# Optimization experiments

Measured on AMD Instinct MI355X. Metric: run time of the kernel, lower is better.

## Reference

```python
import jax, jax.numpy as jnp
import numpy as np

N = 20000      # nodes
E = 320000     # edges per metapath graph
M = 3          # metapaths
IN = 256       # input feat dim
HID = 64       # num_hidden per head
NH = 4         # nhead (layer 1)
OUT = 256      # out_dim
NHO = 1        # nhead_out (layer 2)
SA_H = 128     # semantic attention hidden
NEG_SLOPE = 0.2


def gat_conv(h, W, attn_l, attn_r, src, dst, apply_relu):
    # h: [N, F_in]; W: [F_in, H*D]; attn_l/attn_r: [H, D]
    H, D = attn_l.shape
    feat = (h @ W).reshape(N, H, D)                      # [N, H, D]
    el = jnp.sum(feat * attn_l, axis=-1)                 # [N, H]
    er = jnp.sum(feat * attn_r, axis=-1)                 # [N, H]
    e = jax.nn.leaky_relu(el[src] + er[dst], NEG_SLOPE)  # [E, H]
    # edge softmax grouped by destination node
    emax = jax.ops.segment_max(e, dst, num_segments=N)   # [N, H] (-inf for empty)
    emax = jnp.where(jnp.isfinite(emax), emax, 0.0)
    ee = jnp.exp(e - emax[dst])                          # [E, H]
    denom = jax.ops.segment_sum(ee, dst, num_segments=N) # [N, H]
    alpha = ee / (denom[dst] + 1e-9)                     # [E, H]
    msg = alpha[:, :, None] * feat[src]                  # [E, H, D]
    out = jax.ops.segment_sum(msg, dst, num_segments=N)  # [N, H, D]
    out = out.reshape(N, H * D)                          # concat heads
    return jax.nn.relu(out) if apply_relu else out


def semantic_attention(z, W1, b1, v):
    # z: [N, M, F]
    w = jnp.tanh(z @ W1 + b1) @ v          # [N, M, 1]
    w = w.mean(axis=0)                     # [M, 1]
    beta = jax.nn.softmax(w, axis=0)       # [M, 1]
    out = jnp.sum(beta[None, :, :] * z, axis=1)  # [N, F]
    att_mp = beta.squeeze()                # [M]
    return out, att_mp


def setup_inputs() -> dict:
    key = jax.random.key(0)
    ks = jax.random.split(key, 16)
    s = 0.05
    return {
        "x": jax.random.normal(ks[0], (N, IN), dtype=jnp.float32),
        "edges": jax.random.randint(ks[1], (M, 2, E), 0, N, dtype=jnp.int64)
                 if jax.config.jax_enable_x64 else
                 jax.random.randint(ks[1], (M, 2, E), 0, N, dtype=jnp.int32),
        "W1": jax.random.normal(ks[2], (IN, NH * HID), dtype=jnp.float32) * s,
        "al1": jax.random.normal(ks[3], (NH, HID), dtype=jnp.float32) * s,
        "ar1": jax.random.normal(ks[4], (NH, HID), dtype=jnp.float32) * s,
        "saW1": jax.random.normal(ks[5], (NH * HID, SA_H), dtype=jnp.float32) * s,
        "sab1": jnp.zeros((SA_H,), dtype=jnp.float32),
        "sav1": jax.random.normal(ks[6], (SA_H, 1), dtype=jnp.float32) * s,
        "W2": jax.random.normal(ks[7], (NH * HID, NHO * OUT), dtype=jnp.float32) * s,
        "al2": jax.random.normal(ks[8], (NHO, OUT), dtype=jnp.float32) * s,
        "ar2": jax.random.normal(ks[9], (NHO, OUT), dtype=jnp.float32) * s,
        "saW2": jax.random.normal(ks[10], (NHO * OUT, SA_H), dtype=jnp.float32) * s,
        "sab2": jnp.zeros((SA_H,), dtype=jnp.float32),
        "sav2": jax.random.normal(ks[11], (SA_H, 1), dtype=jnp.float32) * s,
    }


def reference(x, edges, W1, al1, ar1, saW1, sab1, sav1,
              W2, al2, ar2, saW2, sab2, sav2):
    h = x
    # HAN layer 1: shared GATConv over each metapath graph, relu activation
    z = jnp.stack([gat_conv(h, W1, al1, ar1, edges[i, 0], edges[i, 1], True)
                   for i in range(M)], axis=1)          # [N, M, NH*HID]
    h, att_mp = semantic_attention(z, saW1, sab1, sav1)
    # HAN layer 2: last layer, no activation (encoding=False)
    z = jnp.stack([gat_conv(h, W2, al2, ar2, edges[i, 0], edges[i, 1], False)
                   for i in range(M)], axis=1)          # [N, M, NHO*OUT]
    h, att_mp = semantic_attention(z, saW2, sab2, sav2)
    return h, att_mp
```

## Files before the change

### kernel.cpp

```cpp
#include <hip/hip_runtime.h>
#include <hip/hip_bf16.h>
#include <math.h>

#define NN 20000
#define EE 320000
#define MM 3
#define FW 256
#define SAH 128
#define NB 79

typedef __attribute__((ext_vector_type(8))) short bf16x8;
typedef __attribute__((ext_vector_type(4))) float f32x4;

static __device__ __forceinline__ float lrelu(float x){ return x > 0.f ? x : 0.2f*x; }

static __device__ __forceinline__ unsigned short f2bf(float f) {
    unsigned u = __float_as_uint(f);
    return (unsigned short)((u + 0x7FFFu + ((u >> 16) & 1u)) >> 16);
}
static __device__ __forceinline__ float bflo(unsigned u){ return __uint_as_float(u << 16); }
static __device__ __forceinline__ float bfhi(unsigned u){ return __uint_as_float(u & 0xffff0000u); }
static __device__ __forceinline__ unsigned pk2bf(float lo, float hi) {
    return ((unsigned)f2bf(lo)) | (((unsigned)f2bf(hi)) << 16);
}

#define XBLK 2500
__global__ __launch_bounds__(256) void prep_kernel(const float* __restrict__ x, unsigned short* __restrict__ xb,
                                                   const float* __restrict__ W1, unsigned short* __restrict__ W1t,
                                                   const float* __restrict__ saW1, unsigned short* __restrict__ saW1t,
                                                   const float* __restrict__ W2, unsigned short* __restrict__ W2t,
                                                   const float* __restrict__ saW2, unsigned short* __restrict__ saW2t) {
    int b = blockIdx.x, tid = threadIdx.x;
    if (b < XBLK) {
        int i = b*256 + tid;
        const float4* p = (const float4*)x + (size_t)i*2;
        float4 v0 = p[0], v1 = p[1];
        uint4 o;
        o.x = pk2bf(v0.x, v0.y); o.y = pk2bf(v0.z, v0.w);
        o.z = pk2bf(v1.x, v1.y); o.w = pk2bf(v1.z, v1.w);
        ((uint4*)xb)[i] = o;
        return;
    }
    int b2 = b - XBLK;
    if (b2 < 256)      { int n = b2;       W1t  [(size_t)n*256 + tid] = f2bf(W1  [(size_t)tid*256 + n]); }
    else if (b2 < 384) { int n = b2 - 256; saW1t[(size_t)n*256 + tid] = f2bf(saW1[(size_t)tid*SAH + n]); }
    else if (b2 < 640) { int n = b2 - 384; W2t  [(size_t)n*256 + tid] = f2bf(W2  [(size_t)tid*256 + n]); }
    else               { int n = b2 - 640; saW2t[(size_t)n*256 + tid] = f2bf(saW2[(size_t)tid*SAH + n]); }
}

__global__ __launch_bounds__(256) void hist_kernel(const int* __restrict__ edges, int* __restrict__ cnt) {
    int idx = blockIdx.x*256 + threadIdx.x;
    if (idx >= MM*EE/4) return;
    int m = idx / (EE/4), e4 = idx - m*(EE/4);
    int4 d = ((const int4*)(edges + (size_t)(m*2+1)*EE))[e4];
    atomicAdd(&cnt[m*NN + d.x], 1);
    atomicAdd(&cnt[m*NN + d.y], 1);
    atomicAdd(&cnt[m*NN + d.z], 1);
    atomicAdd(&cnt[m*NN + d.w], 1);
}

__global__ __launch_bounds__(256) void scanA_kernel(const int* __restrict__ cnt, int* __restrict__ rowptr, int* __restrict__ bsum) {
    int m = blockIdx.y;
    int i = blockIdx.x*256 + threadIdx.x;
    int v = (i < NN) ? cnt[m*NN + i] : 0;
    int lane = threadIdx.x & 63;
    int val = v;
    #pragma unroll
    for (int o = 1; o < 64; o <<= 1) { int t = __shfl_up(val, o); if (lane >= o) val += t; }
    __shared__ int ws[4];
    int w = threadIdx.x >> 6;
    if (lane == 63) ws[w] = val;
    __syncthreads();
    #pragma unroll
    for (int j = 0; j < 3; ++j) if (j < w) val += ws[j];
    if (i < NN) rowptr[m*(NN+1) + 1 + i] = val;
    if (threadIdx.x == 255) bsum[m*NB + blockIdx.x] = val;
}

__global__ __launch_bounds__(128) void scanB_kernel(const int* __restrict__ bsum, int* __restrict__ boff) {
    __shared__ int s[128];
    int t = threadIdx.x;
    for (int m = 0; m < MM; ++m) {
        int v = (t < NB) ? bsum[m*NB + t] : 0;
        s[t] = v; __syncthreads();
        for (int o = 1; o < 128; o <<= 1) {
            int x = (t >= o) ? s[t - o] : 0;
            __syncthreads();
            s[t] += x;
            __syncthreads();
        }
        if (t < NB) boff[m*NB + t] = s[t] - v;
        __syncthreads();
    }
}

__global__ __launch_bounds__(256) void scanC_kernel(const int* __restrict__ cnt, int* __restrict__ rowptr,
                                                    const int* __restrict__ boff, int* __restrict__ cursor) {
    int m = blockIdx.y;
    int i = blockIdx.x*256 + threadIdx.x;
    if (i >= NN) return;
    int incl = rowptr[m*(NN+1) + 1 + i] + boff[m*NB + blockIdx.x];
    rowptr[m*(NN+1) + 1 + i] = incl;
    cursor[m*NN + i] = incl - cnt[m*NN + i];
    if (i == 0 && blockIdx.x == 0) rowptr[m*(NN+1)] = 0;
}

__global__ __launch_bounds__(256) void scatter_kernel(const int* __restrict__ edges, int* __restrict__ cursor,
                                                      uint2* __restrict__ csr) {
    int idx = blockIdx.x*256 + threadIdx.x;
    if (idx >= MM*EE/4) return;
    int m = idx / (EE/4), e4 = idx - m*(EE/4);
    int4 s = ((const int4*)(edges + (size_t)(m*2  )*EE))[e4];
    int4 d = ((const int4*)(edges + (size_t)(m*2+1)*EE))[e4];
    int p0 = atomicAdd(&cursor[m*NN + d.x], 1); csr[(size_t)m*EE + p0] = make_uint2((unsigned)s.x, (unsigned)d.x);
    int p1 = atomicAdd(&cursor[m*NN + d.y], 1); csr[(size_t)m*EE + p1] = make_uint2((unsigned)s.y, (unsigned)d.y);
    int p2 = atomicAdd(&cursor[m*NN + d.z], 1); csr[(size_t)m*EE + p2] = make_uint2((unsigned)s.z, (unsigned)d.z);
    int p3 = atomicAdd(&cursor[m*NN + d.w], 1); csr[(size_t)m*EE + p3] = make_uint2((unsigned)s.w, (unsigned)d.w);
}

template<int H>
__global__ __launch_bounds__(256) void gemm_mfma_kernel(const unsigned short* __restrict__ A,
                                                        const unsigned short* __restrict__ Bt,
                                                        const float* __restrict__ attl, const float* __restrict__ attr,
                                                        unsigned short* __restrict__ C,
                                                        float* __restrict__ el, float* __restrict__ er) {
    int tid = threadIdx.x;
    int w = tid >> 6, lane = tid & 63;
    int rowgrp = w & 1, half = w >> 1;
    int r0 = blockIdx.x*32 + rowgrp*16;
    int colbase = half * 128;
    int lrow = lane & 15, lk = lane >> 4;

    bf16x8 a[8];
    const unsigned short* ap = A + (size_t)(r0 + lrow)*256 + lk*8;
    #pragma unroll
    for (int k = 0; k < 8; ++k) a[k] = *(const bf16x8*)(ap + k*32);

    float pelv[2][4] = {{0.f,0.f,0.f,0.f},{0.f,0.f,0.f,0.f}};
    float perv[2][4] = {{0.f,0.f,0.f,0.f},{0.f,0.f,0.f,0.f}};

    #pragma unroll
    for (int n = 0; n < 8; ++n) {
        int col0 = colbase + n*16;
        const unsigned short* bp = Bt + (size_t)(col0 + lrow)*256 + lk*8;
        f32x4 acc = {0.f, 0.f, 0.f, 0.f};
        #pragma unroll
        for (int k = 0; k < 8; ++k) {
            bf16x8 bfr = *(const bf16x8*)(bp + k*32);
            acc = __builtin_amdgcn_mfma_f32_16x16x32_bf16(a[k], bfr, acc, 0, 0, 0);
        }
        int col = col0 + lrow;
        float al = attl[col], ar = attr[col];
        int hl = (H == 4) ? (n >> 2) : 0;
        #pragma unroll
        for (int r = 0; r < 4; ++r) {
            float cv = acc[r];
            pelv[hl][r] += cv * al;
            perv[hl][r] += cv * ar;
            C[(size_t)(r0 + lk*4 + r)*256 + col] = f2bf(cv);
        }
    }

    int nhl = (H == 4) ? 2 : 1;
    #pragma unroll
    for (int hl = 0; hl < 2; ++hl) {
        if (hl >= nhl) break;
        #pragma unroll
        for (int r = 0; r < 4; ++r) {
            float pe = pelv[hl][r], pr = perv[hl][r];
            #pragma unroll
            for (int o = 1; o < 16; o <<= 1) { pe += __shfl_xor(pe, o); pr += __shfl_xor(pr, o); }
            pelv[hl][r] = pe; perv[hl][r] = pr;
        }
    }

    if (H == 4) {
        if (lrow == 0) {
            int row = r0 + lk*4;
            #pragma unroll
            for (int hl = 0; hl < 2; ++hl) {
                int head = half*2 + hl;
                #pragma unroll
                for (int r = 0; r < 4; ++r) {
                    el[(size_t)(row + r)*4 + head] = pelv[hl][r];
                    er[(size_t)(row + r)*4 + head] = perv[hl][r];
                }
            }
        }
    } else {
        __shared__ float elds[2][32], erds[2][32];
        if (lrow == 0) {
            int rib = rowgrp*16 + lk*4;
            #pragma unroll
            for (int r = 0; r < 4; ++r) {
                elds[half][rib + r] = pelv[0][r];
                erds[half][rib + r] = perv[0][r];
            }
        }
        __syncthreads();
        if (tid < 32) {
            el[blockIdx.x*32 + tid] = elds[0][tid] + elds[1][tid];
            er[blockIdx.x*32 + tid] = erds[0][tid] + erds[1][tid];
        }
    }
}

template<int H>
__global__ __launch_bounds__(256) void edge_ee_kernel(const uint2* __restrict__ csr,
                                                      const float* __restrict__ el, const float* __restrict__ er,
                                                      float* __restrict__ ee) {
    int idx = blockIdx.x*256 + threadIdx.x;
    if (idx >= MM*EE) return;
    uint2 sd = csr[idx];
    int src = sd.x, dst = sd.y;
    if (H == 4) {
        float4 l = *(const float4*)&el[src*4];
        float4 r = *(const float4*)&er[dst*4];
        float4 s;
        s.x = expf(lrelu(l.x + r.x));
        s.y = expf(lrelu(l.y + r.y));
        s.z = expf(lrelu(l.z + r.z));
        s.w = expf(lrelu(l.w + r.w));
        *(float4*)&ee[(size_t)idx*4] = s;
    } else {
        ee[idx] = expf(lrelu(el[src] + er[dst]));
    }
}

template<int H, bool RELU>
__global__ __launch_bounds__(256) void agg_kernel(const unsigned short* __restrict__ feat,
                                                  const float* __restrict__ ee,
                                                  const int* __restrict__ rowptr,
                                                  const uint2* __restrict__ csr,
                                                  unsigned short* __restrict__ z) {
    int m = blockIdx.y;
    int tid = threadIdx.x;
    int lane = tid & 63, wv = tid >> 6;
    int n = blockIdx.x * 4 + wv;
    int eslot = lane >> 5, flane = lane & 31;
    int h = (H == 4) ? (flane >> 3) : 0;
    int beg = rowptr[m*(NN+1) + n], end = rowptr[m*(NN+1) + n + 1];
    const int eb = m*EE;

    float a[8] = {};
    float den = 0.f;
    int e0 = beg + eslot;

    int   sA = 0, sB = 0;
    float wA = 0.f, wB = 0.f;
    if (e0 < end)     { sA = csr[(size_t)eb+e0  ].x; wA = (H==4)? ee[(size_t)(eb+e0  )*4+h] : ee[eb+e0  ]; }
    if (e0 + 2 < end) { sB = csr[(size_t)eb+e0+2].x; wB = (H==4)? ee[(size_t)(eb+e0+2)*4+h] : ee[eb+e0+2]; }

    for (int e = e0; e < end; e += 2) {
        uint4 v = *(const uint4*)(feat + (size_t)sA*256 + flane*8);
        float w = wA;
        sA = sB; wA = wB;
        if (e + 4 < end) {
            sB = csr[(size_t)eb+e+4].x;
            wB = (H==4)? ee[(size_t)(eb+e+4)*4+h] : ee[eb+e+4];
        }
        den += w;
        a[0] += w * bflo(v.x); a[1] += w * bfhi(v.x);
        a[2] += w * bflo(v.y); a[3] += w * bfhi(v.y);
        a[4] += w * bflo(v.z); a[5] += w * bfhi(v.z);
        a[6] += w * bflo(v.w); a[7] += w * bfhi(v.w);
    }

    #pragma unroll
    for (int j = 0; j < 8; ++j) a[j] += __shfl_xor(a[j], 32);
    den += __shfl_xor(den, 32);

    if (eslot == 0) {
        float inv = 1.f / (den + 1e-9f);
        #pragma unroll
        for (int j = 0; j < 8; ++j) {
            a[j] *= inv;
            if (RELU) a[j] = fmaxf(a[j], 0.f);
        }
        uint4 pk;
        pk.x = pk2bf(a[0], a[1]);
        pk.y = pk2bf(a[2], a[3]);
        pk.z = pk2bf(a[4], a[5]);
        pk.w = pk2bf(a[6], a[7]);
        *(uint4*)&z[((size_t)n*MM + m)*256 + flane*8] = pk;
    }
}

__global__ __launch_bounds__(256) void semw_mfma_kernel(const unsigned short* __restrict__ Z,
                                                        const unsigned short* __restrict__ Wt,
                                                        const float* __restrict__ bias, const float* __restrict__ v,
                                                        float* __restrict__ wsum) {
    int tid = threadIdx.x;
    int w = tid >> 6, lane = tid & 63;
    int r0 = blockIdx.x*64 + w*16;
    int lrow = lane & 15, lk = lane >> 4;

    int arow = r0 + lrow;
    if (arow >= NN*MM) arow = NN*MM - 1;
    bf16x8 a[8];
    const unsigned short* ap = Z + (size_t)arow*256 + lk*8;
    #pragma unroll
    for (int k = 0; k < 8; ++k) a[k] = *(const bf16x8*)(ap + k*32);

    float p[4] = {0.f, 0.f, 0.f, 0.f};
    #pragma unroll
    for (int n = 0; n < 8; ++n) {
        int col = n*16 + lrow;
        const unsigned short* bp = Wt + (size_t)col*256 + lk*8;
        f32x4 acc = {0.f, 0.f, 0.f, 0.f};
        #pragma unroll
        for (int k = 0; k < 8; ++k) {
            bf16x8 bfr = *(const bf16x8*)(bp + k*32);
            acc = __builtin_amdgcn_mfma_f32_16x16x32_bf16(a[k], bfr, acc, 0, 0, 0);
        }
        float bb = bias[col], vv = v[col];
        #pragma unroll
        for (int r = 0; r < 4; ++r)
            p[r] += tanhf(acc[r] + bb) * vv;
    }

    #pragma unroll
    for (int r = 0; r < 4; ++r) {
        #pragma unroll
        for (int o = 1; o < 16; o <<= 1) p[r] += __shfl_xor(p[r], o);
    }

    __shared__ float loc[3];
    if (tid < 3) loc[tid] = 0.f;
    __syncthreads();
    if (lrow == 0) {
        #pragma unroll
        for (int r = 0; r < 4; ++r) {
            int row = r0 + lk*4 + r;
            if (row < NN*MM) atomicAdd(&loc[row % MM], p[r]);
        }
    }
    __syncthreads();
    if (tid < 3) atomicAdd(&wsum[tid], loc[tid]);
}

__global__ void beta_kernel(const float* __restrict__ wsum, float* __restrict__ beta, float* att_out) {
    if (threadIdx.x == 0 && blockIdx.x == 0) {
        float w0 = wsum[0] / (float)NN, w1 = wsum[1] / (float)NN, w2 = wsum[2] / (float)NN;
        float mx = fmaxf(w0, fmaxf(w1, w2));
        float e0 = expf(w0 - mx), e1 = expf(w1 - mx), e2 = expf(w2 - mx);
        float s = e0 + e1 + e2;
        beta[0] = e0 / s; beta[1] = e1 / s; beta[2] = e2 / s;
        if (att_out) { att_out[0] = e0/s; att_out[1] = e1/s; att_out[2] = e2/s; }
    }
}

__global__ __launch_bounds__(128) void combine_bf16_kernel(const unsigned short* __restrict__ z, const float* __restrict__ beta,
                                                           unsigned short* __restrict__ outb) {
    int n = blockIdx.x, t = threadIdx.x;
    float b0 = beta[0], b1 = beta[1], b2 = beta[2];
    size_t base = (size_t)n*MM*256 + t*2;
    unsigned z0 = *(const unsigned*)&z[base];
    unsigned z1 = *(const unsigned*)&z[base + 256];
    unsigned z2 = *(const unsigned*)&z[base + 512];
    float ox = b0*bflo(z0) + b1*bflo(z1) + b2*bflo(z2);
    float oy = b0*bfhi(z0) + b1*bfhi(z1) + b2*bfhi(z2);
    *(unsigned*)&outb[(size_t)n*256 + t*2] = pk2bf(ox, oy);
}

__global__ __launch_bounds__(128) void combine_kernel(const unsigned short* __restrict__ z, const float* __restrict__ beta,
                                                      float* __restrict__ out) {
    int n = blockIdx.x, t = threadIdx.x;
    float b0 = beta[0], b1 = beta[1], b2 = beta[2];
    size_t base = (size_t)n*MM*256 + t*2;
    unsigned z0 = *(const unsigned*)&z[base];
    unsigned z1 = *(const unsigned*)&z[base + 256];
    unsigned z2 = *(const unsigned*)&z[base + 512];
    float2 o;
    o.x = b0*bflo(z0) + b1*bflo(z1) + b2*bflo(z2);
    o.y = b0*bfhi(z0) + b1*bfhi(z1) + b2*bfhi(z2);
    *(float2*)&out[(size_t)n*256 + t*2] = o;
}

extern "C" void kernel_launch(void* const* d_in, const int* in_sizes, int n_in,
                              void* d_out, int out_size, void* d_ws, size_t ws_size,
                              hipStream_t stream) {
    const float* x    = (const float*)d_in[0];
    const int*   edges= (const int*)  d_in[1];
    const float* W1   = (const float*)d_in[2];
    const float* al1  = (const float*)d_in[3];
    const float* ar1  = (const float*)d_in[4];
    const float* saW1 = (const float*)d_in[5];
    const float* sab1 = (const float*)d_in[6];
    const float* sav1 = (const float*)d_in[7];
    const float* W2   = (const float*)d_in[8];
    const float* al2  = (const float*)d_in[9];
    const float* ar2  = (const float*)d_in[10];
    const float* saW2 = (const float*)d_in[11];
    const float* sab2 = (const float*)d_in[12];
    const float* sav2 = (const float*)d_in[13];
    float* out = (float*)d_out;

    char* ws = (char*)d_ws;
    size_t off = 0;
    auto alloc = [&](size_t bytes) { void* p = ws + off; off += (bytes + 255) & ~(size_t)255; return p; };
    unsigned short* feat  = (unsigned short*)alloc((size_t)NN*256*2);
    unsigned short* z     = (unsigned short*)alloc((size_t)NN*MM*256*2);
    unsigned short* xb    = (unsigned short*)alloc((size_t)NN*256*2);
    unsigned short* W1t   = (unsigned short*)alloc(256*256*2);
    unsigned short* saW1t = (unsigned short*)alloc(SAH*256*2);
    unsigned short* W2t   = (unsigned short*)alloc(256*256*2);
    unsigned short* saW2t = (unsigned short*)alloc(SAH*256*2);
    float* ee     = (float*)alloc((size_t)MM*EE*4*4);
    float* el     = (float*)alloc(NN*4*4);
    float* er     = (float*)alloc(NN*4*4);
    float* wsum   = (float*)alloc(256);
    float* beta   = (float*)alloc(256);
    int*   cnt    = (int*)alloc(MM*NN*4);
    int*   cursor = (int*)alloc(MM*NN*4);
    int*   rowptr = (int*)alloc(MM*(NN+1)*4);
    uint2* csr    = (uint2*)alloc((size_t)MM*EE*8);
    int*   bsum   = (int*)alloc(MM*NB*4);
    int*   boff   = (int*)alloc(MM*NB*4);
    unsigned short* hb = xb;

    int egrid = (MM*EE + 255)/256;
    int egrid4 = (MM*EE/4 + 255)/256;
    dim3 sg(NB, MM);

    prep_kernel<<<XBLK + 768, 256, 0, stream>>>(x, xb, W1, W1t, saW1, saW1t, W2, W2t, saW2, saW2t);

    hipMemsetAsync(cnt, 0, MM*NN*4, stream);
    hist_kernel<<<egrid4, 256, 0, stream>>>(edges, cnt);
    scanA_kernel<<<sg, 256, 0, stream>>>(cnt, rowptr, bsum);
    scanB_kernel<<<1, 128, 0, stream>>>(bsum, boff);
    scanC_kernel<<<sg, 256, 0, stream>>>(cnt, rowptr, boff, cursor);
    scatter_kernel<<<egrid4, 256, 0, stream>>>(edges, cursor, csr);

    gemm_mfma_kernel<4><<<NN/32, 256, 0, stream>>>(xb, W1t, al1, ar1, feat, el, er);
    edge_ee_kernel<4><<<egrid, 256, 0, stream>>>(csr, el, er, ee);
    agg_kernel<4, true><<<dim3(NN/4, MM), 256, 0, stream>>>(feat, ee, rowptr, csr, z);
    hipMemsetAsync(wsum, 0, 16, stream);
    semw_mfma_kernel<<<(NN*MM + 63)/64, 256, 0, stream>>>(z, saW1t, sab1, sav1, wsum);
    beta_kernel<<<1, 64, 0, stream>>>(wsum, beta, nullptr);
    combine_bf16_kernel<<<NN, 128, 0, stream>>>(z, beta, hb);

    gemm_mfma_kernel<1><<<NN/32, 256, 0, stream>>>(hb, W2t, al2, ar2, feat, el, er);
    edge_ee_kernel<1><<<egrid, 256, 0, stream>>>(csr, el, er, ee);
    agg_kernel<1, false><<<dim3(NN/4, MM), 256, 0, stream>>>(feat, ee, rowptr, csr, z);
    hipMemsetAsync(wsum, 0, 16, stream);
    semw_mfma_kernel<<<(NN*MM + 63)/64, 256, 0, stream>>>(z, saW2t, sab2, sav2, wsum);
    beta_kernel<<<1, 64, 0, stream>>>(wsum, beta, out + (size_t)NN*256);
    combine_kernel<<<NN, 128, 0, stream>>>(z, beta, out);
}
```

Before: 402.5 us.

## Store CSR as src-only, partition scatter by dst range, make edge_ee per-node

The CSR array now stores only source indices instead of (src,dst) pairs, which halves its memory traffic. The scatter kernel is split into 8 destination ranges so that each block's atomics and writes hit a narrower region and get better locality. This costs reading the edge list 8 times. The edge-weight kernel now walks each destination node's row, loading er once per node instead of once per edge. Warps can be underutilized because the average degree is only 16 while each wave has 64 lanes.

```diff
diff --git a/kernel.cpp b/kernel.cpp
--- a/kernel.cpp
+++ b/kernel.cpp
@@ -8,6 +8,7 @@
 #define FW 256
 #define SAH 128
 #define NB 79
+#define RNG 2500
 
 typedef __attribute__((ext_vector_type(8))) short bf16x8;
 typedef __attribute__((ext_vector_type(4))) float f32x4;
@@ -106,16 +107,19 @@
 }
 
 __global__ __launch_bounds__(256) void scatter_kernel(const int* __restrict__ edges, int* __restrict__ cursor,
-                                                      uint2* __restrict__ csr) {
-    int idx = blockIdx.x*256 + threadIdx.x;
-    if (idx >= MM*EE/4) return;
-    int m = idx / (EE/4), e4 = idx - m*(EE/4);
+                                                      int* __restrict__ csr_src) {
+    int m = blockIdx.y;
+    int r = blockIdx.x & 7;
+    int chunk = blockIdx.x >> 3;
+    int e4 = chunk*256 + threadIdx.x;
+    if (e4 >= EE/4) return;
+    int lo = r * RNG, hi = lo + RNG;
     int4 s = ((const int4*)(edges + (size_t)(m*2  )*EE))[e4];
     int4 d = ((const int4*)(edges + (size_t)(m*2+1)*EE))[e4];
-    int p0 = atomicAdd(&cursor[m*NN + d.x], 1); csr[(size_t)m*EE + p0] = make_uint2((unsigned)s.x, (unsigned)d.x);
-    int p1 = atomicAdd(&cursor[m*NN + d.y], 1); csr[(size_t)m*EE + p1] = make_uint2((unsigned)s.y, (unsigned)d.y);
-    int p2 = atomicAdd(&cursor[m*NN + d.z], 1); csr[(size_t)m*EE + p2] = make_uint2((unsigned)s.z, (unsigned)d.z);
-    int p3 = atomicAdd(&cursor[m*NN + d.w], 1); csr[(size_t)m*EE + p3] = make_uint2((unsigned)s.w, (unsigned)d.w);
+    if (d.x >= lo && d.x < hi) { int p = atomicAdd(&cursor[m*NN + d.x], 1); csr_src[(size_t)m*EE + p] = s.x; }
+    if (d.y >= lo && d.y < hi) { int p = atomicAdd(&cursor[m*NN + d.y], 1); csr_src[(size_t)m*EE + p] = s.y; }
+    if (d.z >= lo && d.z < hi) { int p = atomicAdd(&cursor[m*NN + d.z], 1); csr_src[(size_t)m*EE + p] = s.z; }
+    if (d.w >= lo && d.w < hi) { int p = atomicAdd(&cursor[m*NN + d.w], 1); csr_src[(size_t)m*EE + p] = s.w; }
 }
 
 template<int H>
@@ -206,24 +210,34 @@
 }
 
 template<int H>
-__global__ __launch_bounds__(256) void edge_ee_kernel(const uint2* __restrict__ csr,
+__global__ __launch_bounds__(256) void edge_ee_kernel(const int* __restrict__ csr_src,
+                                                      const int* __restrict__ rowptr,
                                                       const float* __restrict__ el, const float* __restrict__ er,
                                                       float* __restrict__ ee) {
-    int idx = blockIdx.x*256 + threadIdx.x;
-    if (idx >= MM*EE) return;
-    uint2 sd = csr[idx];
-    int src = sd.x, dst = sd.y;
+    int m = blockIdx.y;
+    int tid = threadIdx.x;
+    int lane = tid & 63, wv = tid >> 6;
+    int n = blockIdx.x*4 + wv;
+    int beg = rowptr[m*(NN+1) + n], end = rowptr[m*(NN+1) + n + 1];
+    const int eb = m*EE;
     if (H == 4) {
-        float4 l = *(const float4*)&el[src*4];
-        float4 r = *(const float4*)&er[dst*4];
-        float4 s;
-        s.x = expf(lrelu(l.x + r.x));
-        s.y = expf(lrelu(l.y + r.y));
-        s.z = expf(lrelu(l.z + r.z));
-        s.w = expf(lrelu(l.w + r.w));
-        *(float4*)&ee[(size_t)idx*4] = s;
+        float4 r4 = *(const float4*)&er[n*4];
+        for (int e = beg + lane; e < end; e += 64) {
+            int src = csr_src[eb + e];
+            float4 l = *(const float4*)&el[src*4];
+            float4 s;
+            s.x = expf(lrelu(l.x + r4.x));
+            s.y = expf(lrelu(l.y + r4.y));
+            s.z = expf(lrelu(l.z + r4.z));
+            s.w = expf(lrelu(l.w + r4.w));
+            *(float4*)&ee[(size_t)(eb + e)*4] = s;
+        }
     } else {
-        ee[idx] = expf(lrelu(el[src] + er[dst]));
+        float rn = er[n];
+        for (int e = beg + lane; e < end; e += 64) {
+            int src = csr_src[eb + e];
+            ee[eb + e] = expf(lrelu(el[src] + rn));
+        }
     }
 }
 
@@ -231,7 +245,7 @@
 __global__ __launch_bounds__(256) void agg_kernel(const unsigned short* __restrict__ feat,
                                                   const float* __restrict__ ee,
                                                   const int* __restrict__ rowptr,
-                                                  const uint2* __restrict__ csr,
+                                                  const int* __restrict__ csr_src,
                                                   unsigned short* __restrict__ z) {
     int m = blockIdx.y;
     int tid = threadIdx.x;
@@ -248,15 +262,15 @@
 
     int   sA = 0, sB = 0;
     float wA = 0.f, wB = 0.f;
-    if (e0 < end)     { sA = csr[(size_t)eb+e0  ].x; wA = (H==4)? ee[(size_t)(eb+e0  )*4+h] : ee[eb+e0  ]; }
-    if (e0 + 2 < end) { sB = csr[(size_t)eb+e0+2].x; wB = (H==4)? ee[(size_t)(eb+e0+2)*4+h] : ee[eb+e0+2]; }
+    if (e0 < end)     { sA = csr_src[eb+e0  ]; wA = (H==4)? ee[(size_t)(eb+e0  )*4+h] : ee[eb+e0  ]; }
+    if (e0 + 2 < end) { sB = csr_src[eb+e0+2]; wB = (H==4)? ee[(size_t)(eb+e0+2)*4+h] : ee[eb+e0+2]; }
 
     for (int e = e0; e < end; e += 2) {
         uint4 v = *(const uint4*)(feat + (size_t)sA*256 + flane*8);
         float w = wA;
         sA = sB; wA = wB;
         if (e + 4 < end) {
-            sB = csr[(size_t)eb+e+4].x;
+            sB = csr_src[eb+e+4];
             wB = (H==4)? ee[(size_t)(eb+e+4)*4+h] : ee[eb+e+4];
         }
         den += w;
@@ -414,13 +428,13 @@
     int*   cnt    = (int*)alloc(MM*NN*4);
     int*   cursor = (int*)alloc(MM*NN*4);
     int*   rowptr = (int*)alloc(MM*(NN+1)*4);
-    uint2* csr    = (uint2*)alloc((size_t)MM*EE*8);
+    int*   csr_s  = (int*)alloc((size_t)MM*EE*4);
     int*   bsum   = (int*)alloc(MM*NB*4);
     int*   boff   = (int*)alloc(MM*NB*4);
     unsigned short* hb = xb;
 
-    int egrid = (MM*EE + 255)/256;
     int egrid4 = (MM*EE/4 + 255)/256;
+    int chunks = (EE/4 + 255)/256;
     dim3 sg(NB, MM);
 
     prep_kernel<<<XBLK + 768, 256, 0, stream>>>(x, xb, W1, W1t, saW1, saW1t, W2, W2t, saW2, saW2t);
@@ -430,19 +444,19 @@
     scanA_kernel<<<sg, 256, 0, stream>>>(cnt, rowptr, bsum);
     scanB_kernel<<<1, 128, 0, stream>>>(bsum, boff);
     scanC_kernel<<<sg, 256, 0, stream>>>(cnt, rowptr, boff, cursor);
-    scatter_kernel<<<egrid4, 256, 0, stream>>>(edges, cursor, csr);
+    scatter_kernel<<<dim3(chunks*8, MM), 256, 0, stream>>>(edges, cursor, csr_s);
 
     gemm_mfma_kernel<4><<<NN/32, 256, 0, stream>>>(xb, W1t, al1, ar1, feat, el, er);
-    edge_ee_kernel<4><<<egrid, 256, 0, stream>>>(csr, el, er, ee);
-    agg_kernel<4, true><<<dim3(NN/4, MM), 256, 0, stream>>>(feat, ee, rowptr, csr, z);
+    edge_ee_kernel<4><<<dim3(NN/4, MM), 256, 0, stream>>>(csr_s, rowptr, el, er, ee);
+    agg_kernel<4, true><<<dim3(NN/4, MM), 256, 0, stream>>>(feat, ee, rowptr, csr_s, z);
     hipMemsetAsync(wsum, 0, 16, stream);
     semw_mfma_kernel<<<(NN*MM + 63)/64, 256, 0, stream>>>(z, saW1t, sab1, sav1, wsum);
     beta_kernel<<<1, 64, 0, stream>>>(wsum, beta, nullptr);
     combine_bf16_kernel<<<NN, 128, 0, stream>>>(z, beta, hb);
 
     gemm_mfma_kernel<1><<<NN/32, 256, 0, stream>>>(hb, W2t, al2, ar2, feat, el, er);
-    edge_ee_kernel<1><<<egrid, 256, 0, stream>>>(csr, el, er, ee);
-    agg_kernel<1, false><<<dim3(NN/4, MM), 256, 0, stream>>>(feat, ee, rowptr, csr, z);
+    edge_ee_kernel<1><<<dim3(NN/4, MM), 256, 0, stream>>>(csr_s, rowptr, el, er, ee);
+    agg_kernel<1, false><<<dim3(NN/4, MM), 256, 0, stream>>>(feat, ee, rowptr, csr_s, z);
     hipMemsetAsync(wsum, 0, 16, stream);
     semw_mfma_kernel<<<(NN*MM + 63)/64, 256, 0, stream>>>(z, saW2t, sab2, sav2, wsum);
     beta_kernel<<<1, 64, 0, stream>>>(wsum, beta, out + (size_t)NN*256);
```

Measured after the change: 409.6 us. About the same (+1.8%).
